# Performance work log

Measured on AMD Instinct MI355X. Metric: run time of the kernel, lower is better.

Reference implementation:

```python
import jax, jax.numpy as jnp
import numpy as np
from jax import lax

SELECTION_SIZE = 2  # top-k experts per token


def setup_inputs() -> dict:
    key = jax.random.key(0)
    k1, k2, k3, k4 = jax.random.split(key, 4)
    N, E, IN, OUT = 8192, 8, 2048, 2048
    X = jax.random.normal(k1, (N, IN), dtype=jnp.float32)
    G = jax.random.normal(k2, (N, E), dtype=jnp.float32)
    # expert Linear params: y = x @ W_e.T + b_e, W_e: [out, in]
    W = jax.random.normal(k3, (E, OUT, IN), dtype=jnp.float32) * (1.0 / np.sqrt(IN))
    b = jax.random.normal(k4, (E, OUT), dtype=jnp.float32) * 0.01
    return {"X": X, "G": G, "W": W, "b": b}


def reference(X, G, W, b):
    # softmax gating over experts, then top-k selection and renormalization
    raw_weights = jax.nn.softmax(G, axis=1)                      # [N, E]
    top_w, top_idx = lax.top_k(raw_weights, SELECTION_SIZE)      # [N, k]
    norm_w = top_w / jnp.sum(top_w, axis=1, keepdims=True)       # [N, k]

    # dense all-expert GEMM (same math as per-expert gathered matmuls)
    all_Y = jnp.einsum('ni,eoi->neo', X, W) + b[None, :, :]      # [N, E, out]

    # gather the top-k experts' outputs per token and combine
    sel_Y = jnp.take_along_axis(all_Y, top_idx[:, :, None], axis=1)  # [N, k, out]
    Y = jnp.einsum('nk,nko->no', norm_w, sel_Y)                  # [N, out]
    return Y
```

## Files before the change

### kernel.cpp

```cpp
#include <hip/hip_runtime.h>
#include <hip/hip_bf16.h>

#define N_TOK 8192
#define N_EXP 8
#define DIM_IN 2048
#define DIM_OUT 2048

#define BM 256
#define BN 256
#define BK 64
#define NKT (DIM_IN / BK)

#define NX_ELEMS (N_TOK * DIM_IN)
#define NW_ELEMS (N_EXP * DIM_OUT * DIM_IN)
#define NX_CHUNK (NX_ELEMS / 8)
#define NW_CHUNK_PER_E (NW_ELEMS / 8 / N_EXP)

typedef __attribute__((ext_vector_type(8))) short bf16x8_t;
typedef __attribute__((ext_vector_type(8))) short s16x8_t;
typedef __attribute__((ext_vector_type(4))) short s16x4_t;
typedef __attribute__((ext_vector_type(4))) float f32x4_t;

__device__ __forceinline__ short f2bf(float f) {
    union { __hip_bfloat16 h; short s; } u;
    u.h = __float2bfloat16(f);
    return u.s;
}

__device__ __forceinline__ float bf2f(unsigned short s) {
    union { float f; unsigned u; } v;
    v.u = ((unsigned)s) << 16;
    return v.f;
}

__device__ __forceinline__ void gload_lds16(const void* g, void* l) {
    __builtin_amdgcn_global_load_lds(
        (const __attribute__((address_space(1))) void*)g,
        (__attribute__((address_space(3))) void*)l, 16, 0, 0);
}

__device__ __forceinline__ void cvt8(const float* __restrict__ src,
                                     unsigned short* __restrict__ dst) {
    f32x4_t a = __builtin_nontemporal_load((const f32x4_t*)src);
    f32x4_t b = __builtin_nontemporal_load((const f32x4_t*)(src + 4));
    s16x8_t h;
    h[0] = f2bf(a[0]); h[1] = f2bf(a[1]); h[2] = f2bf(a[2]); h[3] = f2bf(a[3]);
    h[4] = f2bf(b[0]); h[5] = f2bf(b[1]); h[6] = f2bf(b[2]); h[7] = f2bf(b[3]);
    *(s16x8_t*)dst = h;
}

__global__ void moe_zero_kernel(float4* __restrict__ y, int n4, int* __restrict__ counts) {
    int i = blockIdx.x * blockDim.x + threadIdx.x;
    if (i < N_EXP) counts[i] = 0;
    float4 z; z.x = 0.f; z.y = 0.f; z.z = 0.f; z.w = 0.f;
    for (; i < n4; i += gridDim.x * blockDim.x) y[i] = z;
}

__global__ void moe_gate_cvt_kernel(const float* __restrict__ G,
                                    const float* __restrict__ X, const float* __restrict__ W,
                                    int* __restrict__ counts,
                                    int* __restrict__ lists, float* __restrict__ lw,
                                    int* __restrict__ slotA, int* __restrict__ slotB,
                                    float* __restrict__ wAo, float* __restrict__ wBo,
                                    unsigned short* __restrict__ Xb, unsigned short* __restrict__ Wb) {
    const int t = blockIdx.x * blockDim.x + threadIdx.x;
    if (t < N_TOK) {
        float g[N_EXP];
#pragma unroll
        for (int e = 0; e < N_EXP; ++e) g[e] = G[t * N_EXP + e];
        int i0 = 0; float b0 = g[0];
#pragma unroll
        for (int e = 1; e < N_EXP; ++e) if (g[e] > b0) { b0 = g[e]; i0 = e; }
        int i1 = -1; float b1 = -INFINITY;
#pragma unroll
        for (int e = 0; e < N_EXP; ++e) if (e != i0 && g[e] > b1) { b1 = g[e]; i1 = e; }
        float e1 = expf(b1 - b0);
        float w0 = 1.0f / (1.0f + e1);
        float w1 = e1 * w0;
        int p0 = atomicAdd(&counts[i0], 1);
        lists[i0 * N_TOK + p0] = t;
        lw[i0 * N_TOK + p0] = w0;
        int p1 = atomicAdd(&counts[i1], 1);
        lists[i1 * N_TOK + p1] = t;
        lw[i1 * N_TOK + p1] = w1;
        slotA[t] = (i0 << 13) | p0;
        slotB[t] = (i1 << 13) | p1;
        wAo[t] = w0;
        wBo[t] = w1;
    }
    for (int i = blockIdx.x * blockDim.x + threadIdx.x; i < NX_CHUNK;
         i += gridDim.x * blockDim.x) {
        cvt8(X + (size_t)i * 8, Xb + (size_t)i * 8);
    }
    {
        const int e = blockIdx.x & 7;
        const int bslot = blockIdx.x >> 3;
        const size_t ebase = (size_t)e * NW_CHUNK_PER_E;
#pragma unroll
        for (int p = 0; p < 8; ++p) {
            size_t ic = (size_t)bslot * 2048 + p * 256 + threadIdx.x;
            size_t off = (ebase + ic) * 8;
            cvt8(W + off, Wb + off);
        }
    }
}

__global__ void moe_gate_kernel(const float* __restrict__ G,
                                int* __restrict__ counts,
                                int* __restrict__ lists,
                                float* __restrict__ lw,
                                int* __restrict__ slotA, int* __restrict__ slotB,
                                float* __restrict__ wAo, float* __restrict__ wBo) {
    int t = blockIdx.x * blockDim.x + threadIdx.x;
    if (t >= N_TOK) return;
    float g[N_EXP];
#pragma unroll
    for (int e = 0; e < N_EXP; ++e) g[e] = G[t * N_EXP + e];
    int i0 = 0; float b0 = g[0];
#pragma unroll
    for (int e = 1; e < N_EXP; ++e) if (g[e] > b0) { b0 = g[e]; i0 = e; }
    int i1 = -1; float b1 = -INFINITY;
#pragma unroll
    for (int e = 0; e < N_EXP; ++e) if (e != i0 && g[e] > b1) { b1 = g[e]; i1 = e; }
    float e1 = expf(b1 - b0);
    float w0 = 1.0f / (1.0f + e1);
    float w1 = e1 * w0;
    int p0 = atomicAdd(&counts[i0], 1);
    lists[i0 * N_TOK + p0] = t;
    lw[i0 * N_TOK + p0] = w0;
    int p1 = atomicAdd(&counts[i1], 1);
    lists[i1 * N_TOK + p1] = t;
    lw[i1 * N_TOK + p1] = w1;
    slotA[t] = (i0 << 13) | p0;
    slotB[t] = (i1 << 13) | p1;
    wAo[t] = w0;
    wBo[t] = w1;
}

__global__ __launch_bounds__(256) void moe_combine_kernel(
        const unsigned short* __restrict__ scratch, const int* __restrict__ counts,
        const int* __restrict__ slotA, const int* __restrict__ slotB,
        const float* __restrict__ wA, const float* __restrict__ wB,
        float* __restrict__ Y) {
    const int c = threadIdx.x * 8;
    int cnt[N_EXP];
#pragma unroll
    for (int i = 0; i < N_EXP; ++i) cnt[i] = counts[i];
#pragma unroll
    for (int s = 0; s < 2; ++s) {
        const int t = blockIdx.x * 2 + s;
        const int sa = slotA[t];
        const int sb = slotB[t];
        const int eA = sa >> 13, eB = sb >> 13;
        int baseA = 0, baseB = 0;
#pragma unroll
        for (int i = 0; i < N_EXP; ++i) {
            baseA += (i < eA) ? cnt[i] : 0;
            baseB += (i < eB) ? cnt[i] : 0;
        }
        const long gA = baseA + (sa & 8191);
        const long gB = baseB + (sb & 8191);
        const float wa = wA[t], wb = wB[t];
        s16x8_t a = __builtin_nontemporal_load((const s16x8_t*)(scratch + gA * DIM_OUT + c));
        s16x8_t b = __builtin_nontemporal_load((const s16x8_t*)(scratch + gB * DIM_OUT + c));
        f32x4_t y0, y1;
#pragma unroll
        for (int j = 0; j < 4; ++j) {
            y0[j] = wa * bf2f((unsigned short)a[j])     + wb * bf2f((unsigned short)b[j]);
            y1[j] = wa * bf2f((unsigned short)a[j + 4]) + wb * bf2f((unsigned short)b[j + 4]);
        }
        f32x4_t* y = (f32x4_t*)(Y + (long)t * DIM_OUT + c);
        __builtin_nontemporal_store(y0, y);
        __builtin_nontemporal_store(y1, y + 1);
    }
}

__global__ __launch_bounds__(512, 2) void moe_gemm_bf16(
        const unsigned short* __restrict__ Xb, const unsigned short* __restrict__ Wb,
        const float* __restrict__ bias,
        const int* __restrict__ counts, const int* __restrict__ lists,
        const float* __restrict__ lw,
        unsigned short* __restrict__ scratch, float* __restrict__ Y) {
    const int L = blockIdx.x + (DIM_OUT / BN) * (blockIdx.y + (N_TOK / BM) * blockIdx.z);
    const int e = L & 7;
    const int idx = L >> 3;
    const int M = counts[e];
    const int m0 = (idx >> 3) * BM;
    if (m0 >= M) return;
    int vr = M - m0; if (vr > BM) vr = BM;
    const int col0 = (idx & 7) * BN;

    __shared__ unsigned short As[2][BM * BK];
    __shared__ unsigned short Bs[2][BN * BK];

    const int tid = threadIdx.x;
    const int lane = tid & 63;
    const int wid = tid >> 6;
    const int wn = (wid & 3) * 64;

    const int* mylist = lists + e * N_TOK + m0;
    const float* lwp = lw + e * N_TOK + m0;

    const int srow = tid >> 3;
    const int scol = ((tid & 7) ^ (srow & 7)) * 8;

    const unsigned short* bptr = Wb + ((size_t)e * DIM_OUT + col0 + srow) * DIM_IN + scol;

    const int ldsbase = wid * 512;

    const int rl = lane & 15;
    const int hi = lane >> 4;
    const char* AsC = (const char*)As;
    const char* BsC = (const char*)Bs;

#define STAGE_B_H(buf, h, koff)                                                 \
    do {                                                                        \
        _Pragma("unroll")                                                       \
        for (int i = 2 * (h); i < 2 * (h) + 2; ++i)                             \
            gload_lds16(bptr + (size_t)(i * 64) * DIM_IN + (koff),              \
                        &Bs[buf][i * 4096 + ldsbase]);                          \
    } while (0)

    if (vr > 128) {
        const int wm = (wid >> 2) * 128;

        const unsigned short* aptr[4];
#pragma unroll
        for (int i = 0; i < 4; ++i) {
            int r = srow + 64 * i;
            int tok = (m0 + r < M) ? mylist[r] : mylist[0];
            aptr[i] = Xb + (size_t)tok * DIM_IN + scol;
        }

        unsigned vA[2], vB[2];
#pragma unroll
        for (int kk = 0; kk < 2; ++kk) {
            unsigned x = (unsigned)(((kk << 6) | (hi << 4)) ^ ((rl & 7) << 4));
            vA[kk] = (unsigned)((wm + rl) * 128) + x;
            vB[kk] = (unsigned)((wn + rl) * 128) + x;
        }

        f32x4_t acc[8][4];
#pragma unroll
        for (int m = 0; m < 8; ++m)
#pragma unroll
            for (int n = 0; n < 4; ++n)
                acc[m][n] = (f32x4_t)(0.0f);

#define STAGE_A_H(buf, h, koff)                                                 \
    do {                                                                        \
        _Pragma("unroll")                                                       \
        for (int i = 2 * (h); i < 2 * (h) + 2; ++i)                             \
            gload_lds16(aptr[i] + (koff), &As[buf][i * 4096 + ldsbase]);        \
    } while (0)

        STAGE_A_H(0, 0, 0);  STAGE_A_H(0, 1, 0);  STAGE_B_H(0, 0, 0);  STAGE_B_H(0, 1, 0);
        STAGE_A_H(1, 0, BK); STAGE_A_H(1, 1, BK); STAGE_B_H(1, 0, BK);

#define DO_TILE(CC, KOFN, KOF2)                                                 \
    {                                                                           \
        asm volatile("s_waitcnt vmcnt(6)" ::: "memory");                        \
        __builtin_amdgcn_s_barrier();                                           \
        asm volatile("" ::: "memory");                                          \
        STAGE_B_H(1 - (CC), 1, (KOFN));                                         \
        bf16x8_t bfr[4][2], af0[4][2], af1[4][2];                               \
        _Pragma("unroll")                                                       \
        for (int n = 0; n < 4; ++n)                                             \
            _Pragma("unroll")                                                   \
            for (int kk = 0; kk < 2; ++kk)                                      \
                bfr[n][kk] = *(const bf16x8_t*)(BsC + vB[kk] + ((CC) * 32768 + n * 2048)); \
        _Pragma("unroll")                                                       \
        for (int m = 0; m < 4; ++m)                                             \
            _Pragma("unroll")                                                   \
            for (int kk = 0; kk < 2; ++kk)                                      \
                af0[m][kk] = *(const bf16x8_t*)(AsC + vA[kk] + ((CC) * 32768 + m * 2048)); \
        __builtin_amdgcn_s_setprio(1);                                          \
        _Pragma("unroll")                                                       \
        for (int m = 0; m < 2; ++m)                                             \
            _Pragma("unroll")                                                   \
            for (int n = 0; n < 4; ++n)                                         \
                _Pragma("unroll")                                               \
                for (int kk = 0; kk < 2; ++kk)                                  \
                    acc[m][n] = __builtin_amdgcn_mfma_f32_16x16x32_bf16(af0[m][kk], bfr[n][kk], acc[m][n], 0, 0, 0); \
        __builtin_amdgcn_s_setprio(0);                                          \
        _Pragma("unroll")                                                       \
        for (int m = 0; m < 4; ++m)                                             \
            _Pragma("unroll")                                                   \
            for (int kk = 0; kk < 2; ++kk)                                      \
                af1[m][kk] = *(const bf16x8_t*)(AsC + vA[kk] + ((CC) * 32768 + (m + 4) * 2048)); \
        __builtin_amdgcn_s_setprio(1);                                          \
        _Pragma("unroll")                                                       \
        for (int m = 2; m < 4; ++m)                                             \
            _Pragma("unroll")                                                   \
            for (int n = 0; n < 4; ++n)                                         \
                _Pragma("unroll")                                               \
                for (int kk = 0; kk < 2; ++kk)                                  \
                    acc[m][n] = __builtin_amdgcn_mfma_f32_16x16x32_bf16(af0[m][kk], bfr[n][kk], acc[m][n], 0, 0, 0); \
        __builtin_amdgcn_s_setprio(0);                                          \
        asm volatile("s_waitcnt lgkmcnt(0)" ::: "memory");                      \
        __builtin_amdgcn_sched_barrier(0);                                      \
        __builtin_amdgcn_s_barrier();                                           \
        asm volatile("" ::: "memory");                                          \
        STAGE_A_H((CC), 0, (KOF2));                                             \
        __builtin_amdgcn_s_setprio(1);                                          \
        _Pragma("unroll")                                                       \
        for (int m = 0; m < 2; ++m)                                             \
            _Pragma("unroll")                                                   \
            for (int n = 0; n < 4; ++n)                                         \
                _Pragma("unroll")                                               \
                for (int kk = 0; kk < 2; ++kk)                                  \
                    acc[m + 4][n] = __builtin_amdgcn_mfma_f32_16x16x32_bf16(af1[m][kk], bfr[n][kk], acc[m + 4][n], 0, 0, 0); \
        __builtin_amdgcn_s_setprio(0);                                          \
        STAGE_A_H((CC), 1, (KOF2));                                             \
        __builtin_amdgcn_s_setprio(1);                                          \
        _Pragma("unroll")                                                       \
        for (int n = 0; n < 4; ++n)                                             \
            _Pragma("unroll")                                                   \
            for (int kk = 0; kk < 2; ++kk)                                      \
                acc[6][n] = __builtin_amdgcn_mfma_f32_16x16x32_bf16(af1[2][kk], bfr[n][kk], acc[6][n], 0, 0, 0); \
        __builtin_amdgcn_s_setprio(0);                                          \
        STAGE_B_H((CC), 0, (KOF2));                                             \
        __builtin_amdgcn_s_setprio(1);                                          \
        _Pragma("unroll")                                                       \
        for (int n = 0; n < 4; ++n)                                             \
            _Pragma("unroll")                                                   \
            for (int kk = 0; kk < 2; ++kk)                                      \
                acc[7][n] = __builtin_amdgcn_mfma_f32_16x16x32_bf16(af1[3][kk], bfr[n][kk], acc[7][n], 0, 0, 0); \
        __builtin_amdgcn_s_setprio(0);                                          \
    }

        for (int kt = 0; kt < NKT; kt += 2) {
            const int kofn0 = (kt + 1) * BK;
            const int kof20 = ((kt + 2 < NKT) ? (kt + 2) : (NKT - 1)) * BK;
            const int kofn1 = kof20;
            const int kof21 = ((kt + 3 < NKT) ? (kt + 3) : (NKT - 1)) * BK;
            DO_TILE(0, kofn0, kof20)
            DO_TILE(1, kofn1, kof21)
        }
        asm volatile("s_waitcnt vmcnt(0)" ::: "memory");

        const int cl = lane & 15;
        const int rq = (lane >> 4) << 2;
        float biasv[4];
#pragma unroll
        for (int n = 0; n < 4; ++n) biasv[n] = bias[e * DIM_OUT + col0 + wn + n * 16 + cl];

        if (scratch) {
            int segbase = m0;
            for (int i = 0; i < e; ++i) segbase += counts[i];
#pragma unroll
            for (int m = 0; m < 8; ++m) {
#pragma unroll
                for (int j = 0; j < 4; ++j) {
                    int row = wm + (m << 4) + rq + j;
                    if (m0 + row < M) {
                        short* out = (short*)(scratch + (size_t)(segbase + row) * DIM_OUT + col0 + wn);
#pragma unroll
                        for (int n = 0; n < 4; ++n)
                            __builtin_nontemporal_store(f2bf(acc[m][n][j] + biasv[n]), out + n * 16 + cl);
                    }
                }
            }
        } else {
#pragma unroll
            for (int m = 0; m < 8; ++m) {
#pragma unroll
                for (int j = 0; j < 4; ++j) {
                    int row = wm + (m << 4) + rq + j;
                    if (m0 + row < M) {
                        int tok = mylist[row];
                        float wgt = lwp[row];
                        float* yrow = Y + (size_t)tok * DIM_OUT + col0 + wn;
#pragma unroll
                        for (int n = 0; n < 4; ++n)
                            atomicAdd(yrow + n * 16 + cl, wgt * (acc[m][n][j] + biasv[n]));
                    }
                }
            }
        }
    } else {
        const int wm = (wid >> 2) * 64;

        const unsigned short* aptrT[2];
#pragma unroll
        for (int i = 0; i < 2; ++i) {
            int r = srow + 64 * i;
            int tok = (m0 + r < M) ? mylist[r] : mylist[0];
            aptrT[i] = Xb + (size_t)tok * DIM_IN + scol;
        }

        unsigned vA[2], vB[2];
#pragma unroll
        for (int kk = 0; kk < 2; ++kk) {
            unsigned x = (unsigned)(((kk << 6) | (hi << 4)) ^ ((rl & 7) << 4));
            vA[kk] = (unsigned)((wm + rl) * 128) + x;
            vB[kk] = (unsigned)((wn + rl) * 128) + x;
        }

        f32x4_t acc[4][4];
#pragma unroll
        for (int m = 0; m < 4; ++m)
#pragma unroll
            for (int n = 0; n < 4; ++n)
                acc[m][n] = (f32x4_t)(0.0f);

#define STAGE_A_T(buf, koff)                                                    \
    do {                                                                        \
        _Pragma("unroll")                                                       \
        for (int i = 0; i < 2; ++i)                                             \
            gload_lds16(aptrT[i] + (koff), &As[buf][i * 4096 + ldsbase]);       \
    } while (0)

        STAGE_A_T(0, 0);  STAGE_B_H(0, 0, 0);  STAGE_B_H(0, 1, 0);
        STAGE_A_T(1, BK); STAGE_B_H(1, 0, BK);

#define DO_TILE_T(CC, KOFN, KOF2)                                               \
    {                                                                           \
        asm volatile("s_waitcnt vmcnt(4)" ::: "memory");                        \
        __builtin_amdgcn_s_barrier();                                           \
        asm volatile("" ::: "memory");                                          \
        STAGE_B_H(1 - (CC), 1, (KOFN));                                         \
        bf16x8_t bfr[4][2], af[4][2];                                           \
        _Pragma("unroll")                                                       \
        for (int n = 0; n < 4; ++n)                                             \
            _Pragma("unroll")                                                   \
            for (int kk = 0; kk < 2; ++kk)                                      \
                bfr[n][kk] = *(const bf16x8_t*)(BsC + vB[kk] + ((CC) * 32768 + n * 2048)); \
        _Pragma("unroll")                                                       \
        for (int m = 0; m < 4; ++m)                                             \
            _Pragma("unroll")                                                   \
            for (int kk = 0; kk < 2; ++kk)                                      \
                af[m][kk] = *(const bf16x8_t*)(AsC + vA[kk] + ((CC) * 32768 + m * 2048)); \
        __builtin_amdgcn_s_setprio(1);                                          \
        _Pragma("unroll")                                                       \
        for (int m = 0; m < 2; ++m)                                             \
            _Pragma("unroll")                                                   \
            for (int n = 0; n < 4; ++n)                                         \
                _Pragma("unroll")                                               \
                for (int kk = 0; kk < 2; ++kk)                                  \
                    acc[m][n] = __builtin_amdgcn_mfma_f32_16x16x32_bf16(af[m][kk], bfr[n][kk], acc[m][n], 0, 0, 0); \
        __builtin_amdgcn_s_setprio(0);                                          \
        asm volatile("s_waitcnt lgkmcnt(0)" ::: "memory");                      \
        __builtin_amdgcn_sched_barrier(0);                                      \
        __builtin_amdgcn_s_barrier();                                           \
        asm volatile("" ::: "memory");                                          \
        STAGE_A_T((CC), (KOF2));                                                \
        __builtin_amdgcn_s_setprio(1);                                          \
        _Pragma("unroll")                                                       \
        for (int m = 2; m < 4; ++m)                                             \
            _Pragma("unroll")                                                   \
            for (int n = 0; n < 4; ++n)                                         \
                _Pragma("unroll")                                               \
                for (int kk = 0; kk < 2; ++kk)                                  \
                    acc[m][n] = __builtin_amdgcn_mfma_f32_16x16x32_bf16(af[m][kk], bfr[n][kk], acc[m][n], 0, 0, 0); \
        __builtin_amdgcn_s_setprio(0);                                          \
        STAGE_B_H((CC), 0, (KOF2));                                             \
    }

        for (int kt = 0; kt < NKT; kt += 2) {
            const int kofn0 = (kt + 1) * BK;
            const int kof20 = ((kt + 2 < NKT) ? (kt + 2) : (NKT - 1)) * BK;
            const int kofn1 = kof20;
            const int kof21 = ((kt + 3 < NKT) ? (kt + 3) : (NKT - 1)) * BK;
            DO_TILE_T(0, kofn0, kof20)
            DO_TILE_T(1, kofn1, kof21)
        }
        asm volatile("s_waitcnt vmcnt(0)" ::: "memory");

        const int cl = lane & 15;
        const int rq = (lane >> 4) << 2;
        float biasv[4];
#pragma unroll
        for (int n = 0; n < 4; ++n) biasv[n] = bias[e * DIM_OUT + col0 + wn + n * 16 + cl];

        if (scratch) {
            int segbase = m0;
            for (int i = 0; i < e; ++i) segbase += counts[i];
#pragma unroll
            for (int m = 0; m < 4; ++m) {
#pragma unroll
                for (int j = 0; j < 4; ++j) {
                    int row = wm + (m << 4) + rq + j;
                    if (m0 + row < M) {
                        short* out = (short*)(scratch + (size_t)(segbase + row) * DIM_OUT + col0 + wn);
#pragma unroll
                        for (int n = 0; n < 4; ++n)
                            __builtin_nontemporal_store(f2bf(acc[m][n][j] + biasv[n]), out + n * 16 + cl);
                    }
                }
            }
        } else {
#pragma unroll
            for (int m = 0; m < 4; ++m) {
#pragma unroll
                for (int j = 0; j < 4; ++j) {
                    int row = wm + (m << 4) + rq + j;
                    if (m0 + row < M) {
                        int tok = mylist[row];
                        float wgt = lwp[row];
                        float* yrow = Y + (size_t)tok * DIM_OUT + col0 + wn;
#pragma unroll
                        for (int n = 0; n < 4; ++n)
                            atomicAdd(yrow + n * 16 + cl, wgt * (acc[m][n][j] + biasv[n]));
                    }
                }
            }
        }
    }
#undef DO_TILE
#undef DO_TILE_T
#undef STAGE_A_H
#undef STAGE_A_T
#undef STAGE_B_H
}

__global__ __launch_bounds__(256, 2) void moe_gemm_f32(
        const float* __restrict__ X, const float* __restrict__ W,
        const float* __restrict__ bias,
        const int* __restrict__ counts, const int* __restrict__ lists,
        const float* __restrict__ lw, float* __restrict__ Y) {
    const int e = blockIdx.z;
    const int M = counts[e];
    const int m0 = blockIdx.y * 128;
    if (m0 >= M) return;
    const int col0 = blockIdx.x * 128;

    __shared__ short As[128 * 64];
    __shared__ short Bs[128 * 64];
    char* Ab = (char*)As;
    char* Bb = (char*)Bs;

    const int tid = threadIdx.x;
    const int lane = tid & 63;
    const int wid = tid >> 6;
    const int wm = (wid >> 1) * 64;
    const int wn = (wid & 1) * 64;

    const int* mylist = lists + e * N_TOK + m0;
    const float* lwp = lw + e * N_TOK + m0;

    const int srow = tid >> 4;
    const int scol = (tid & 15) << 2;
    const int swzW = (srow & 7) << 4;

    const float* xptr[8];
#pragma unroll
    for (int p = 0; p < 8; ++p) {
        int r = p * 16 + srow;
        int tok = (m0 + r < M) ? mylist[r] : mylist[0];
        xptr[p] = X + (size_t)tok * DIM_IN + scol;
    }
    const float* wptr = W + ((size_t)e * DIM_OUT + col0 + srow) * DIM_IN + scol;

    f32x4_t acc[4][4];
#pragma unroll
    for (int m = 0; m < 4; ++m)
#pragma unroll
        for (int n = 0; n < 4; ++n)
            acc[m][n] = (f32x4_t)(0.0f);

    for (int k0 = 0; k0 < DIM_IN; k0 += 64) {
#pragma unroll
        for (int p = 0; p < 8; ++p) {
            int r = p * 16 + srow;
            unsigned byteoff = (unsigned)(r * 128 + scol * 2) ^ swzW;
            float4 va = *(const float4*)(xptr[p] + k0);
            s16x4_t ha; ha[0] = f2bf(va.x); ha[1] = f2bf(va.y); ha[2] = f2bf(va.z); ha[3] = f2bf(va.w);
            *(s16x4_t*)(Ab + byteoff) = ha;
            float4 vb = *(const float4*)(wptr + (size_t)p * 16 * DIM_IN + k0);
            s16x4_t hb; hb[0] = f2bf(vb.x); hb[1] = f2bf(vb.y); hb[2] = f2bf(vb.z); hb[3] = f2bf(vb.w);
            *(s16x4_t*)(Bb + byteoff) = hb;
        }
        __syncthreads();

#pragma unroll
        for (int kk = 0; kk < 2; ++kk) {
            const int kb = (kk << 6) + ((lane >> 4) << 4);
            bf16x8_t af[4], bfr[4];
#pragma unroll
            for (int m = 0; m < 4; ++m) {
                int r = wm + (m << 4) + (lane & 15);
                unsigned byteoff = (unsigned)(r * 128 + kb) ^ ((unsigned)(r & 7) << 4);
                af[m] = *(const bf16x8_t*)(Ab + byteoff);
            }
#pragma unroll
            for (int n = 0; n < 4; ++n) {
                int r = wn + (n << 4) + (lane & 15);
                unsigned byteoff = (unsigned)(r * 128 + kb) ^ ((unsigned)(r & 7) << 4);
                bfr[n] = *(const bf16x8_t*)(Bb + byteoff);
            }
#pragma unroll
            for (int m = 0; m < 4; ++m)
#pragma unroll
                for (int n = 0; n < 4; ++n)
                    acc[m][n] = __builtin_amdgcn_mfma_f32_16x16x32_bf16(af[m], bfr[n], acc[m][n], 0, 0, 0);
        }
        __syncthreads();
    }

    const int cl = lane & 15;
    const int rq = (lane >> 4) << 2;
    float biasv[4];
#pragma unroll
    for (int n = 0; n < 4; ++n) biasv[n] = bias[e * DIM_OUT + col0 + wn + n * 16 + cl];
#pragma unroll
    for (int m = 0; m < 4; ++m) {
#pragma unroll
        for (int j = 0; j < 4; ++j) {
            int row = wm + (m << 4) + rq + j;
            if (m0 + row < M) {
                int tok = mylist[row];
                float wgt = lwp[row];
                float* yrow = Y + (size_t)tok * DIM_OUT + col0 + wn;
#pragma unroll
                for (int n = 0; n < 4; ++n)
                    atomicAdd(yrow + n * 16 + cl, wgt * (acc[m][n][j] + biasv[n]));
            }
        }
    }
}

extern "C" void kernel_launch(void* const* d_in, const int* in_sizes, int n_in,
                              void* d_out, int out_size, void* d_ws, size_t ws_size,
                              hipStream_t stream) {
    const float* X = (const float*)d_in[0];
    const float* G = (const float*)d_in[1];
    const float* W = (const float*)d_in[2];
    const float* b = (const float*)d_in[3];
    float* Y = (float*)d_out;

    char* ws = (char*)d_ws;
    int*   counts = (int*)ws;
    int*   slotA  = (int*)(ws + 256);
    int*   slotB  = (int*)(ws + 256 + 32768);
    float* wA     = (float*)(ws + 256 + 65536);
    float* wB     = (float*)(ws + 256 + 98304);
    int*   lists  = (int*)(ws + 256 + 131072);
    float* lw     = (float*)(ws + 256 + 131072 + 262144);
    size_t o_Xb   = 256 + 131072 + 2 * 262144;
    unsigned short* Xb = (unsigned short*)(ws + o_Xb);
    size_t o_Wb   = o_Xb + (size_t)NX_ELEMS * 2;
    unsigned short* Wb = (unsigned short*)(ws + o_Wb);
    size_t o_scr  = o_Wb + (size_t)NW_ELEMS * 2;
    unsigned short* scratch = (unsigned short*)(ws + o_scr);
    const size_t ws_need_mid  = o_scr;
    const size_t ws_need_full = o_scr + (size_t)2 * N_TOK * DIM_OUT * 2;

    const bool use_scratch = (ws_size >= ws_need_full);
    const bool use_bf16    = (ws_size >= ws_need_mid);

    if (use_bf16) {
        if (use_scratch) {
            hipMemsetAsync(counts, 0, 64, stream);
        } else {
            moe_zero_kernel<<<2048, 256, 0, stream>>>((float4*)Y, out_size / 16, counts);
        }
        moe_gate_cvt_kernel<<<2048, 256, 0, stream>>>(G, X, W, counts, lists, lw,
                                                      slotA, slotB, wA, wB, Xb, Wb);
        dim3 grid(DIM_OUT / BN, N_TOK / BM, N_EXP);
        moe_gemm_bf16<<<grid, 512, 0, stream>>>(Xb, Wb, b, counts, lists, lw,
                                                use_scratch ? scratch : nullptr, Y);
        if (use_scratch) {
            moe_combine_kernel<<<N_TOK / 2, 256, 0, stream>>>(scratch, counts, slotA, slotB,
                                                              wA, wB, Y);
        }
    } else {
        moe_zero_kernel<<<2048, 256, 0, stream>>>((float4*)Y, out_size / 16, counts);
        moe_gate_kernel<<<(N_TOK + 255) / 256, 256, 0, stream>>>(G, counts, lists, lw,
                                                                 slotA, slotB, wA, wB);
        dim3 grid(DIM_OUT / 128, N_TOK / 128, N_EXP);
        moe_gemm_f32<<<grid, 256, 0, stream>>>(X, W, b, counts, lists, lw, Y);
    }
}
```

Baseline: 295.3 us.

## Shrink bf16 MoE GEMM tiles to 128x128 and drop the dual-path tail handling

Reduces the block tile from 256x256 to 128x128 with 512 threads per block, each wave now computing a 64x32 sub-tile, and raises the launch-bounds occupancy hint to 4 blocks per CU. The separate full and tail (vr<=128) code paths are merged into one smaller kernel body with fewer accumulators and shallower staging waits. Smaller tiles cut padding waste on partially filled expert segments and allow more resident blocks, at the cost of less operand reuse per loaded byte and more global/LDS traffic per FLOP. Host-side grid sizing is not shown, so whether the launch dimensions match the new tile mapping is unclear.

```diff
diff --git a/kernel.cpp b/kernel.cpp
--- a/kernel.cpp
+++ b/kernel.cpp
@@ -6,8 +6,8 @@
 #define DIM_IN 2048
 #define DIM_OUT 2048
 
-#define BM 256
-#define BN 256
+#define BM 128
+#define BN 128
 #define BK 64
 #define NKT (DIM_IN / BK)
 
@@ -175,7 +175,7 @@
     }
 }
 
-__global__ __launch_bounds__(512, 2) void moe_gemm_bf16(
+__global__ __launch_bounds__(512, 4) void moe_gemm_bf16(
         const unsigned short* __restrict__ Xb, const unsigned short* __restrict__ Wb,
         const float* __restrict__ bias,
         const int* __restrict__ counts, const int* __restrict__ lists,
@@ -185,10 +185,9 @@
     const int e = L & 7;
     const int idx = L >> 3;
     const int M = counts[e];
-    const int m0 = (idx >> 3) * BM;
+    const int m0 = (idx >> 4) * BM;
     if (m0 >= M) return;
-    int vr = M - m0; if (vr > BM) vr = BM;
-    const int col0 = (idx & 7) * BN;
+    const int col0 = (idx & 15) * BN;
 
     __shared__ unsigned short As[2][BM * BK];
     __shared__ unsigned short Bs[2][BN * BK];
@@ -196,7 +195,8 @@
     const int tid = threadIdx.x;
     const int lane = tid & 63;
     const int wid = tid >> 6;
-    const int wn = (wid & 3) * 64;
+    const int wm = (wid >> 2) * 64;
+    const int wn = (wid & 3) * 32;
 
     const int* mylist = lists + e * N_TOK + m0;
     const float* lwp = lw + e * N_TOK + m0;
@@ -213,229 +213,59 @@
     const char* AsC = (const char*)As;
     const char* BsC = (const char*)Bs;
 
-#define STAGE_B_H(buf, h, koff)                                                 \
-    do {                                                                        \
-        _Pragma("unroll")                                                       \
-        for (int i = 2 * (h); i < 2 * (h) + 2; ++i)                             \
-            gload_lds16(bptr + (size_t)(i * 64) * DIM_IN + (koff),              \
-                        &Bs[buf][i * 4096 + ldsbase]);                          \
-    } while (0)
-
-    if (vr > 128) {
-        const int wm = (wid >> 2) * 128;
-
-        const unsigned short* aptr[4];
-#pragma unroll
-        for (int i = 0; i < 4; ++i) {
-            int r = srow + 64 * i;
-            int tok = (m0 + r < M) ? mylist[r] : mylist[0];
-            aptr[i] = Xb + (size_t)tok * DIM_IN + scol;
-        }
-
-        unsigned vA[2], vB[2];
-#pragma unroll
-        for (int kk = 0; kk < 2; ++kk) {
-            unsigned x = (unsigned)(((kk << 6) | (hi << 4)) ^ ((rl & 7) << 4));
-            vA[kk] = (unsigned)((wm + rl) * 128) + x;
-            vB[kk] = (unsigned)((wn + rl) * 128) + x;
-        }
-
-        f32x4_t acc[8][4];
-#pragma unroll
-        for (int m = 0; m < 8; ++m)
-#pragma unroll
-            for (int n = 0; n < 4; ++n)
-                acc[m][n] = (f32x4_t)(0.0f);
-
-#define STAGE_A_H(buf, h, koff)                                                 \
-    do {                                                                        \
-        _Pragma("unroll")                                                       \
-        for (int i = 2 * (h); i < 2 * (h) + 2; ++i)                             \
-            gload_lds16(aptr[i] + (koff), &As[buf][i * 4096 + ldsbase]);        \
-    } while (0)
-
-        STAGE_A_H(0, 0, 0);  STAGE_A_H(0, 1, 0);  STAGE_B_H(0, 0, 0);  STAGE_B_H(0, 1, 0);
-        STAGE_A_H(1, 0, BK); STAGE_A_H(1, 1, BK); STAGE_B_H(1, 0, BK);
+    const unsigned short* aptr[2];
+#pragma unroll
+    for (int i = 0; i < 2; ++i) {
+        int r = srow + 64 * i;
+        int tok = (m0 + r < M) ? mylist[r] : mylist[0];
+        aptr[i] = Xb + (size_t)tok * DIM_IN + scol;
+    }
+
+    unsigned vA[2], vB[2];
+#pragma unroll
+    for (int kk = 0; kk < 2; ++kk) {
+        unsigned x = (unsigned)(((kk << 6) | (hi << 4)) ^ ((rl & 7) << 4));
+        vA[kk] = (unsigned)((wm + rl) * 128) + x;
+        vB[kk] = (unsigned)((wn + rl) * 128) + x;
+    }
+
+    f32x4_t acc[4][2];
+#pragma unroll
+    for (int m = 0; m < 4; ++m)
+#pragma unroll
+        for (int n = 0; n < 2; ++n)
+            acc[m][n] = (f32x4_t)(0.0f);
+
+#define STAGE_A1(buf, i, koff)                                                  \
+    gload_lds16(aptr[i] + (koff), &As[buf][(i) * 4096 + ldsbase])
+#define STAGE_B1(buf, i, koff)                                                  \
+    gload_lds16(bptr + (size_t)((i) * 64) * DIM_IN + (koff), &Bs[buf][(i) * 4096 + ldsbase])
+
+    STAGE_A1(0, 0, 0);  STAGE_A1(0, 1, 0);  STAGE_B1(0, 0, 0);  STAGE_B1(0, 1, 0);
+    STAGE_A1(1, 0, BK); STAGE_A1(1, 1, BK); STAGE_B1(1, 0, BK);
 
 #define DO_TILE(CC, KOFN, KOF2)                                                 \
     {                                                                           \
-        asm volatile("s_waitcnt vmcnt(6)" ::: "memory");                        \
+        asm volatile("s_waitcnt vmcnt(3)" ::: "memory");                        \
         __builtin_amdgcn_s_barrier();                                           \
         asm volatile("" ::: "memory");                                          \
-        STAGE_B_H(1 - (CC), 1, (KOFN));                                         \
-        bf16x8_t bfr[4][2], af0[4][2], af1[4][2];                               \
+        STAGE_B1(1 - (CC), 1, (KOFN));                                          \
+        bf16x8_t bfr[2][2], af[4][2];                                           \
         _Pragma("unroll")                                                       \
-        for (int n = 0; n < 4; ++n)                                             \
+        for (int n = 0; n < 2; ++n)                                             \
             _Pragma("unroll")                                                   \
             for (int kk = 0; kk < 2; ++kk)                                      \
-                bfr[n][kk] = *(const bf16x8_t*)(BsC + vB[kk] + ((CC) * 32768 + n * 2048)); \
+                bfr[n][kk] = *(const bf16x8_t*)(BsC + vB[kk] + ((CC) * 16384 + n * 2048)); \
         _Pragma("unroll")                                                       \
         for (int m = 0; m < 4; ++m)                                             \
             _Pragma("unroll")                                                   \
             for (int kk = 0; kk < 2; ++kk)                                      \
-                af0[m][kk] = *(const bf16x8_t*)(AsC + vA[kk] + ((CC) * 32768 + m * 2048)); \
+                af[m][kk] = *(const bf16x8_t*)(AsC + vA[kk] + ((CC) * 16384 + m * 2048)); \
         __builtin_amdgcn_s_setprio(1);                                          \
         _Pragma("unroll")                                                       \
         for (int m = 0; m < 2; ++m)                                             \
             _Pragma("unroll")                                                   \
-            for (int n = 0; n < 4; ++n)                                         \
-                _Pragma("unroll")                                               \
-                for (int kk = 0; kk < 2; ++kk)                                  \
-                    acc[m][n] = __builtin_amdgcn_mfma_f32_16x16x32_bf16(af0[m][kk], bfr[n][kk], acc[m][n], 0, 0, 0); \
-        __builtin_amdgcn_s_setprio(0);                                          \
-        _Pragma("unroll")                                                       \
-        for (int m = 0; m < 4; ++m)                                             \
-            _Pragma("unroll")                                                   \
-            for (int kk = 0; kk < 2; ++kk)                                      \
-                af1[m][kk] = *(const bf16x8_t*)(AsC + vA[kk] + ((CC) * 32768 + (m + 4) * 2048)); \
-        __builtin_amdgcn_s_setprio(1);                                          \
-        _Pragma("unroll")                                                       \
-        for (int m = 2; m < 4; ++m)                                             \
-            _Pragma("unroll")                                                   \
-            for (int n = 0; n < 4; ++n)                                         \
-                _Pragma("unroll")                                               \
-                for (int kk = 0; kk < 2; ++kk)                                  \
-                    acc[m][n] = __builtin_amdgcn_mfma_f32_16x16x32_bf16(af0[m][kk], bfr[n][kk], acc[m][n], 0, 0, 0); \
-        __builtin_amdgcn_s_setprio(0);                                          \
-        asm volatile("s_waitcnt lgkmcnt(0)" ::: "memory");                      \
-        __builtin_amdgcn_sched_barrier(0);                                      \
-        __builtin_amdgcn_s_barrier();                                           \
-        asm volatile("" ::: "memory");                                          \
-        STAGE_A_H((CC), 0, (KOF2));                                             \
-        __builtin_amdgcn_s_setprio(1);                                          \
-        _Pragma("unroll")                                                       \
-        for (int m = 0; m < 2; ++m)                                             \
-            _Pragma("unroll")                                                   \
-            for (int n = 0; n < 4; ++n)                                         \
-                _Pragma("unroll")                                               \
-                for (int kk = 0; kk < 2; ++kk)                                  \
-                    acc[m + 4][n] = __builtin_amdgcn_mfma_f32_16x16x32_bf16(af1[m][kk], bfr[n][kk], acc[m + 4][n], 0, 0, 0); \
-        __builtin_amdgcn_s_setprio(0);                                          \
-        STAGE_A_H((CC), 1, (KOF2));                                             \
-        __builtin_amdgcn_s_setprio(1);                                          \
-        _Pragma("unroll")                                                       \
-        for (int n = 0; n < 4; ++n)                                             \
-            _Pragma("unroll")                                                   \
-            for (int kk = 0; kk < 2; ++kk)                                      \
-                acc[6][n] = __builtin_amdgcn_mfma_f32_16x16x32_bf16(af1[2][kk], bfr[n][kk], acc[6][n], 0, 0, 0); \
-        __builtin_amdgcn_s_setprio(0);                                          \
-        STAGE_B_H((CC), 0, (KOF2));                                             \
-        __builtin_amdgcn_s_setprio(1);                                          \
-        _Pragma("unroll")                                                       \
-        for (int n = 0; n < 4; ++n)                                             \
-            _Pragma("unroll")                                                   \
-            for (int kk = 0; kk < 2; ++kk)                                      \
-                acc[7][n] = __builtin_amdgcn_mfma_f32_16x16x32_bf16(af1[3][kk], bfr[n][kk], acc[7][n], 0, 0, 0); \
-        __builtin_amdgcn_s_setprio(0);                                          \
-    }
-
-        for (int kt = 0; kt < NKT; kt += 2) {
-            const int kofn0 = (kt + 1) * BK;
-            const int kof20 = ((kt + 2 < NKT) ? (kt + 2) : (NKT - 1)) * BK;
-            const int kofn1 = kof20;
-            const int kof21 = ((kt + 3 < NKT) ? (kt + 3) : (NKT - 1)) * BK;
-            DO_TILE(0, kofn0, kof20)
-            DO_TILE(1, kofn1, kof21)
-        }
-        asm volatile("s_waitcnt vmcnt(0)" ::: "memory");
-
-        const int cl = lane & 15;
-        const int rq = (lane >> 4) << 2;
-        float biasv[4];
-#pragma unroll
-        for (int n = 0; n < 4; ++n) biasv[n] = bias[e * DIM_OUT + col0 + wn + n * 16 + cl];
-
-        if (scratch) {
-            int segbase = m0;
-            for (int i = 0; i < e; ++i) segbase += counts[i];
-#pragma unroll
-            for (int m = 0; m < 8; ++m) {
-#pragma unroll
-                for (int j = 0; j < 4; ++j) {
-                    int row = wm + (m << 4) + rq + j;
-                    if (m0 + row < M) {
-                        short* out = (short*)(scratch + (size_t)(segbase + row) * DIM_OUT + col0 + wn);
-#pragma unroll
-                        for (int n = 0; n < 4; ++n)
-                            __builtin_nontemporal_store(f2bf(acc[m][n][j] + biasv[n]), out + n * 16 + cl);
-                    }
-                }
-            }
-        } else {
-#pragma unroll
-            for (int m = 0; m < 8; ++m) {
-#pragma unroll
-                for (int j = 0; j < 4; ++j) {
-                    int row = wm + (m << 4) + rq + j;
-                    if (m0 + row < M) {
-                        int tok = mylist[row];
-                        float wgt = lwp[row];
-                        float* yrow = Y + (size_t)tok * DIM_OUT + col0 + wn;
-#pragma unroll
-                        for (int n = 0; n < 4; ++n)
-                            atomicAdd(yrow + n * 16 + cl, wgt * (acc[m][n][j] + biasv[n]));
-                    }
-                }
-            }
-        }
-    } else {
-        const int wm = (wid >> 2) * 64;
-
-        const unsigned short* aptrT[2];
-#pragma unroll
-        for (int i = 0; i < 2; ++i) {
-            int r = srow + 64 * i;
-            int tok = (m0 + r < M) ? mylist[r] : mylist[0];
-            aptrT[i] = Xb + (size_t)tok * DIM_IN + scol;
-        }
-
-        unsigned vA[2], vB[2];
-#pragma unroll
-        for (int kk = 0; kk < 2; ++kk) {
-            unsigned x = (unsigned)(((kk << 6) | (hi << 4)) ^ ((rl & 7) << 4));
-            vA[kk] = (unsigned)((wm + rl) * 128) + x;
-            vB[kk] = (unsigned)((wn + rl) * 128) + x;
-        }
-
-        f32x4_t acc[4][4];
-#pragma unroll
-        for (int m = 0; m < 4; ++m)
-#pragma unroll
-            for (int n = 0; n < 4; ++n)
-                acc[m][n] = (f32x4_t)(0.0f);
-
-#define STAGE_A_T(buf, koff)                                                    \
-    do {                                                                        \
-        _Pragma("unroll")                                                       \
-        for (int i = 0; i < 2; ++i)                                             \
-            gload_lds16(aptrT[i] + (koff), &As[buf][i * 4096 + ldsbase]);       \
-    } while (0)
-
-        STAGE_A_T(0, 0);  STAGE_B_H(0, 0, 0);  STAGE_B_H(0, 1, 0);
-        STAGE_A_T(1, BK); STAGE_B_H(1, 0, BK);
-
-#define DO_TILE_T(CC, KOFN, KOF2)                                               \
-    {                                                                           \
-        asm volatile("s_waitcnt vmcnt(4)" ::: "memory");                        \
-        __builtin_amdgcn_s_barrier();                                           \
-        asm volatile("" ::: "memory");                                          \
-        STAGE_B_H(1 - (CC), 1, (KOFN));                                         \
-        bf16x8_t bfr[4][2], af[4][2];                                           \
-        _Pragma("unroll")                                                       \
-        for (int n = 0; n < 4; ++n)                                             \
-            _Pragma("unroll")                                                   \
-            for (int kk = 0; kk < 2; ++kk)                                      \
-                bfr[n][kk] = *(const bf16x8_t*)(BsC + vB[kk] + ((CC) * 32768 + n * 2048)); \
-        _Pragma("unroll")                                                       \
-        for (int m = 0; m < 4; ++m)                                             \
-            _Pragma("unroll")                                                   \
-            for (int kk = 0; kk < 2; ++kk)                                      \
-                af[m][kk] = *(const bf16x8_t*)(AsC + vA[kk] + ((CC) * 32768 + m * 2048)); \
-        __builtin_amdgcn_s_setprio(1);                                          \
-        _Pragma("unroll")                                                       \
-        for (int m = 0; m < 2; ++m)                                             \
-            _Pragma("unroll")                                                   \
-            for (int n = 0; n < 4; ++n)                                         \
+            for (int n = 0; n < 2; ++n)                                         \
                 _Pragma("unroll")                                               \
                 for (int kk = 0; kk < 2; ++kk)                                  \
                     acc[m][n] = __builtin_amdgcn_mfma_f32_16x16x32_bf16(af[m][kk], bfr[n][kk], acc[m][n], 0, 0, 0); \
@@ -444,74 +274,77 @@
         __builtin_amdgcn_sched_barrier(0);                                      \
         __builtin_amdgcn_s_barrier();                                           \
         asm volatile("" ::: "memory");                                          \
-        STAGE_A_T((CC), (KOF2));                                                \
+        STAGE_A1((CC), 0, (KOF2));                                              \
         __builtin_amdgcn_s_setprio(1);                                          \
         _Pragma("unroll")                                                       \
-        for (int m = 2; m < 4; ++m)                                             \
+        for (int n = 0; n < 2; ++n)                                             \
             _Pragma("unroll")                                                   \
-            for (int n = 0; n < 4; ++n)                                         \
-                _Pragma("unroll")                                               \
-                for (int kk = 0; kk < 2; ++kk)                                  \
-                    acc[m][n] = __builtin_amdgcn_mfma_f32_16x16x32_bf16(af[m][kk], bfr[n][kk], acc[m][n], 0, 0, 0); \
+            for (int kk = 0; kk < 2; ++kk)                                      \
+                acc[2][n] = __builtin_amdgcn_mfma_f32_16x16x32_bf16(af[2][kk], bfr[n][kk], acc[2][n], 0, 0, 0); \
         __builtin_amdgcn_s_setprio(0);                                          \
-        STAGE_B_H((CC), 0, (KOF2));                                             \
-    }
-
-        for (int kt = 0; kt < NKT; kt += 2) {
-            const int kofn0 = (kt + 1) * BK;
-            const int kof20 = ((kt + 2 < NKT) ? (kt + 2) : (NKT - 1)) * BK;
-            const int kofn1 = kof20;
-            const int kof21 = ((kt + 3 < NKT) ? (kt + 3) : (NKT - 1)) * BK;
-            DO_TILE_T(0, kofn0, kof20)
-            DO_TILE_T(1, kofn1, kof21)
-        }
-        asm volatile("s_waitcnt vmcnt(0)" ::: "memory");
-
-        const int cl = lane & 15;
-        const int rq = (lane >> 4) << 2;
-        float biasv[4];
-#pragma unroll
-        for (int n = 0; n < 4; ++n) biasv[n] = bias[e * DIM_OUT + col0 + wn + n * 16 + cl];
-
-        if (scratch) {
-            int segbase = m0;
-            for (int i = 0; i < e; ++i) segbase += counts[i];
-#pragma unroll
-            for (int m = 0; m < 4; ++m) {
-#pragma unroll
-                for (int j = 0; j < 4; ++j) {
-                    int row = wm + (m << 4) + rq + j;
-                    if (m0 + row < M) {
-                        short* out = (short*)(scratch + (size_t)(segbase + row) * DIM_OUT + col0 + wn);
-#pragma unroll
-                        for (int n = 0; n < 4; ++n)
-                            __builtin_nontemporal_store(f2bf(acc[m][n][j] + biasv[n]), out + n * 16 + cl);
-                    }
+        STAGE_A1((CC), 1, (KOF2));                                              \
+        __builtin_amdgcn_s_setprio(1);                                          \
+        _Pragma("unroll")                                                       \
+        for (int n = 0; n < 2; ++n)                                             \
+            _Pragma("unroll")                                                   \
+            for (int kk = 0; kk < 2; ++kk)                                      \
+                acc[3][n] = __builtin_amdgcn_mfma_f32_16x16x32_bf16(af[3][kk], bfr[n][kk], acc[3][n], 0, 0, 0); \
+        __builtin_amdgcn_s_setprio(0);                                          \
+        STAGE_B1((CC), 0, (KOF2));                                              \
+    }
+
+    for (int kt = 0; kt < NKT; kt += 2) {
+        const int kofn0 = (kt + 1) * BK;
+        const int kof20 = ((kt + 2 < NKT) ? (kt + 2) : (NKT - 1)) * BK;
+        const int kofn1 = kof20;
+        const int kof21 = ((kt + 3 < NKT) ? (kt + 3) : (NKT - 1)) * BK;
+        DO_TILE(0, kofn0, kof20)
+        DO_TILE(1, kofn1, kof21)
+    }
+    asm volatile("s_waitcnt vmcnt(0)" ::: "memory");
+#undef DO_TILE
+#undef STAGE_A1
+#undef STAGE_B1
+
+    const int cl = lane & 15;
+    const int rq = (lane >> 4) << 2;
+    float biasv[2];
+#pragma unroll
+    for (int n = 0; n < 2; ++n) biasv[n] = bias[e * DIM_OUT + col0 + wn + n * 16 + cl];
+
+    if (scratch) {
+        int segbase = m0;
+        for (int i = 0; i < e; ++i) segbase += counts[i];
+#pragma unroll
+        for (int m = 0; m < 4; ++m) {
+#pragma unroll
+            for (int j = 0; j < 4; ++j) {
+                int row = wm + (m << 4) + rq + j;
+                if (m0 + row < M) {
+                    short* out = (short*)(scratch + (size_t)(segbase + row) * DIM_OUT + col0 + wn);
+#pragma unroll
+                    for (int n = 0; n < 2; ++n)
+                        __builtin_nontemporal_store(f2bf(acc[m][n][j] + biasv[n]), out + n * 16 + cl);
                 }
             }
-        } else {
-#pragma unroll
-            for (int m = 0; m < 4; ++m) {
-#pragma unroll
-                for (int j = 0; j < 4; ++j) {
-                    int row = wm + (m << 4) + rq + j;
-                    if (m0 + row < M) {
-                        int tok = mylist[row];
-                        float wgt = lwp[row];
-                        float* yrow = Y + (size_t)tok * DIM_OUT + col0 + wn;
-#pragma unroll
-                        for (int n = 0; n < 4; ++n)
-                            atomicAdd(yrow + n * 16 + cl, wgt * (acc[m][n][j] + biasv[n]));
-                    }
+        }
+    } else {
+#pragma unroll
+        for (int m = 0; m < 4; ++m) {
+#pragma unroll
+            for (int j = 0; j < 4; ++j) {
+                int row = wm + (m << 4) + rq + j;
+                if (m0 + row < M) {
+                    int tok = mylist[row];
+                    float wgt = lwp[row];
+                    float* yrow = Y + (size_t)tok * DIM_OUT + col0 + wn;
+#pragma unroll
+                    for (int n = 0; n < 2; ++n)
+                        atomicAdd(yrow + n * 16 + cl, wgt * (acc[m][n][j] + biasv[n]));
                 }
             }
         }
     }
-#undef DO_TILE
-#undef DO_TILE_T
-#undef STAGE_A_H
-#undef STAGE_A_T
-#undef STAGE_B_H
 }
 
 __global__ __launch_bounds__(256, 2) void moe_gemm_f32(
```

New measurement: 307.5 us. 1.04x slower.
